# Kernel tuning notes

Hardware: AMD Instinct MI355X
Metric: run time of the kernel (lower is better)

## Reference

```python
import jax, jax.numpy as jnp
import numpy as np

B, S, D = 4, 2048, 512
H = 8
HD = D // H  # 64


def setup_inputs() -> dict:
    key = jax.random.key(0)
    k1, k2, k3 = jax.random.split(key, 3)
    x = jax.random.normal(k1, (B, S, D), dtype=jnp.float32)
    w_qkv = jax.random.normal(k2, (3 * D, D), dtype=jnp.float32) * (D ** -0.5)
    w_out = jax.random.normal(k3, (D, D), dtype=jnp.float32) * (D ** -0.5)
    return {"x": x, "w_qkv": w_qkv, "w_out": w_out}


def reference(x, w_qkv, w_out):
    b, s, d = x.shape
    # qkv projection (no bias), split into q,k,v
    qkv = jnp.einsum('bsd,ed->bse', x, w_qkv)  # [b, s, 3*d]
    q, k, v = jnp.split(qkv, 3, axis=2)
    # [b, s, h*hd] -> [b, h, s, hd]
    def to_heads(t):
        return t.reshape(b, s, H, HD).transpose(0, 2, 1, 3)
    q, k, v = to_heads(q), to_heads(k), to_heads(v)
    # NOTE: original module only scales by sqrt(head_dim) when mask is given;
    # with mask=None softmax is over raw QK^T scores.
    scores = jnp.einsum('bnid,bnjd->bnij', q, k)  # [b, h, s, s]
    attn = jax.nn.softmax(scores, axis=-1)
    o = jnp.einsum('bnij,bnjd->bnid', attn, v)  # [b, h, s, hd]
    o = o.transpose(0, 2, 1, 3).reshape(b, s, d)
    # dropout is identity (eval / drop_prob=0)
    return jnp.einsum('bsd,ed->bse', o, w_out)
```

## Files before the change

kernel.cpp:

```cpp
#include <hip/hip_runtime.h>
#include <hip/hip_bf16.h>

constexpr int B_  = 4;
constexpr int S_  = 2048;
constexpr int D_  = 512;
constexpr int H_  = 8;
constexpr int HD_ = 64;
constexpr int M_  = B_ * S_;

constexpr float LOG2E = 1.4426950408889634f;

typedef __attribute__((ext_vector_type(8))) short short8v;
typedef __attribute__((ext_vector_type(8))) _Float16 half8v;
typedef __attribute__((ext_vector_type(8))) unsigned short ushort8v;
typedef __attribute__((ext_vector_type(4))) float float4v;
typedef __attribute__((ext_vector_type(16))) float float16v;

__device__ __forceinline__ unsigned short f2bf(float x) {
    unsigned u = __builtin_bit_cast(unsigned, x);
    u += 0x7fffu + ((u >> 16) & 1u);
    return (unsigned short)(u >> 16);
}
__device__ __forceinline__ float bf2f(unsigned short h) {
    return __builtin_bit_cast(float, ((unsigned)h) << 16);
}
__device__ __forceinline__ unsigned short f2h(float x) {
    return __builtin_bit_cast(unsigned short, (_Float16)x);
}
__device__ __forceinline__ float fast_exp2(float x) {
#if __has_builtin(__builtin_amdgcn_exp2f)
    return __builtin_amdgcn_exp2f(x);
#else
    return exp2f(x);
#endif
}
__device__ __forceinline__ unsigned pack_bf16_trunc(float lo, float hi) {
    const unsigned ulo = __builtin_bit_cast(unsigned, lo);
    const unsigned uhi = __builtin_bit_cast(unsigned, hi);
#if __has_builtin(__builtin_amdgcn_perm)
    return __builtin_amdgcn_perm(uhi, ulo, 0x07060302u);
#else
    return (uhi & 0xffff0000u) | (ulo >> 16);
#endif
}
__device__ __forceinline__ void gload_lds16(const void* g, void* lds) {
    __builtin_amdgcn_global_load_lds((const __attribute__((address_space(1))) unsigned*)g,
                                     (__attribute__((address_space(3))) unsigned*)lds, 16, 0, 0);
}

__global__ __launch_bounds__(256) void prepass(const float* __restrict__ x,
                                               const float* __restrict__ wqkv,
                                               const float* __restrict__ wout,
                                               unsigned short* __restrict__ Xp,
                                               unsigned short* __restrict__ Wh,
                                               unsigned short* __restrict__ Wlq,
                                               unsigned short* __restrict__ Wob) {
    const int bid = blockIdx.x, t = threadIdx.x;
    if (bid < 2048) {
        const int flat = bid * 256 + t;
        const int m = flat >> 6, c = (flat & 63) * 8;
        const float4 a = *(const float4*)&x[(size_t)m * 512 + c];
        const float4 b = *(const float4*)&x[(size_t)m * 512 + c + 4];
        const float v[8] = {a.x, a.y, a.z, a.w, b.x, b.y, b.z, b.w};
        ushort8v hi, lo;
#pragma unroll
        for (int i = 0; i < 8; ++i) {
            const unsigned short h = f2bf(v[i]);
            hi[i] = h; lo[i] = f2bf(v[i] - bf2f(h));
        }
        *(ushort8v*)&Xp[(size_t)m * 1024 + c]       = hi;
        *(ushort8v*)&Xp[(size_t)m * 1024 + 512 + c] = lo;
    } else if (bid < 2048 + 384) {
        const int flat = (bid - 2048) * 256 + t;
        const int e = flat >> 6, c = (flat & 63) * 8;
        const float4 a = *(const float4*)&wqkv[(size_t)e * 512 + c];
        const float4 b = *(const float4*)&wqkv[(size_t)e * 512 + c + 4];
        const float v[8] = {a.x, a.y, a.z, a.w, b.x, b.y, b.z, b.w};
        ushort8v hi, lo;
#pragma unroll
        for (int i = 0; i < 8; ++i) {
            const unsigned short h = f2bf(v[i]);
            hi[i] = h; lo[i] = f2bf(v[i] - bf2f(h));
        }
        *(ushort8v*)&Wh[(size_t)e * 512 + c] = hi;
        if (e < 512) *(ushort8v*)&Wlq[(size_t)e * 512 + c] = lo;
    } else {
        const int flat = (bid - 2432) * 256 + t;
        const int e = flat >> 6, c = (flat & 63) * 8;
        const float4 a = *(const float4*)&wout[(size_t)e * 512 + c];
        const float4 b = *(const float4*)&wout[(size_t)e * 512 + c + 4];
        const float v[8] = {a.x, a.y, a.z, a.w, b.x, b.y, b.z, b.w};
        ushort8v hi;
#pragma unroll
        for (int i = 0; i < 8; ++i) hi[i] = f2bf(v[i]);
        *(ushort8v*)&Wob[(size_t)e * 512 + c] = hi;
    }
}

__global__ __launch_bounds__(256, 3) void gemm_qkv(const unsigned short* __restrict__ Xp,
                                                   const unsigned short* __restrict__ Wh,
                                                   const unsigned short* __restrict__ Wlq,
                                                   unsigned short* __restrict__ Qf,
                                                   unsigned short* __restrict__ KH,
                                                   unsigned short* __restrict__ VT) {
    __shared__ unsigned short Asm[2][128 * 64];
    __shared__ unsigned short Bsm[2][64 * 64];
    const int t = threadIdx.x, wv = t >> 6, lane = t & 63;
    const int fm = lane & 15, fq = lane >> 4;
    const int bid0 = blockIdx.x + 24 * blockIdx.y;
    const int xcd = bid0 & 7, ii = bid0 >> 3;
    const int x  = ii % 24;
    const int m0 = ((ii / 24) * 8 + xcd) * 128;
    const int slice = x >> 3;
    const int e0 = (x & 7) * 64;
    const bool vblk = (slice == 2);
    const int kiters = (slice == 0) ? 24 : 8;
    const int wrow = (wv >> 1) * 64, wcol = (wv & 1) * 32;

    const unsigned short* BbaseWh =
        Wh + (size_t)(e0 + (slice == 1 ? 512 : (slice == 2 ? 1024 : 0))) * 512;
    const unsigned short* BbaseWlq = Wlq + (size_t)e0 * 512;

    const int srow = t >> 3;
    const int skb0 = t & 7;

    float4v acc[4][2];
#pragma unroll
    for (int i = 0; i < 4; ++i)
#pragma unroll
        for (int j = 0; j < 2; ++j) acc[i][j] = (float4v){0.f, 0.f, 0.f, 0.f};

    {
#pragma unroll
        for (int i = 0; i < 4; ++i) {
            const int row = srow + 32 * i;
            const int kb = skb0 ^ (row & 7);
            gload_lds16(Xp + (size_t)(m0 + row) * 1024 + kb * 8,
                        &Asm[0][(wv * 64 + 256 * i) * 8]);
        }
#pragma unroll
        for (int i = 0; i < 2; ++i) {
            const int row = srow + 32 * i;
            const int kb = skb0 ^ (row & 7);
            gload_lds16(BbaseWh + (size_t)row * 512 + kb * 8,
                        &Bsm[0][(wv * 64 + 256 * i) * 8]);
        }
    }

    for (int kk = 0; kk < kiters; ++kk) {
        __syncthreads();

        if (kk + 1 < kiters) {
            const int nk = kk + 1;
            const int pass = nk >> 3;
            const int k0n = (nk & 7) * 64;
            const int nbuf = nk & 1;
            const int aoff = (slice == 0 && pass == 1) ? 512 : 0;
            const unsigned short* Bp = (slice == 0 && pass == 2) ? BbaseWlq : BbaseWh;
#pragma unroll
            for (int i = 0; i < 4; ++i) {
                const int row = srow + 32 * i;
                const int kb = skb0 ^ (row & 7);
                gload_lds16(Xp + (size_t)(m0 + row) * 1024 + aoff + k0n + kb * 8,
                            &Asm[nbuf][(wv * 64 + 256 * i) * 8]);
            }
#pragma unroll
            for (int i = 0; i < 2; ++i) {
                const int row = srow + 32 * i;
                const int kb = skb0 ^ (row & 7);
                gload_lds16(Bp + (size_t)row * 512 + k0n + kb * 8,
                            &Bsm[nbuf][(wv * 64 + 256 * i) * 8]);
            }
        }

        const int buf = kk & 1;
#pragma unroll
        for (int ks = 0; ks < 2; ++ks) {
            short8v af[4], bf[2];
#pragma unroll
            for (int mt = 0; mt < 4; ++mt) {
                const int row = wrow + mt * 16 + fm;
                af[mt] = *(const short8v*)&Asm[buf][row * 64 + 8 * ((4 * ks + fq) ^ (row & 7))];
            }
#pragma unroll
            for (int nt = 0; nt < 2; ++nt) {
                const int row = wcol + nt * 16 + fm;
                bf[nt] = *(const short8v*)&Bsm[buf][row * 64 + 8 * ((4 * ks + fq) ^ (row & 7))];
            }
            if (vblk) {
#pragma unroll
                for (int mt = 0; mt < 4; ++mt)
#pragma unroll
                    for (int nt = 0; nt < 2; ++nt)
                        acc[mt][nt] = __builtin_amdgcn_mfma_f32_16x16x32_bf16(bf[nt], af[mt], acc[mt][nt], 0, 0, 0);
            } else {
#pragma unroll
                for (int mt = 0; mt < 4; ++mt)
#pragma unroll
                    for (int nt = 0; nt < 2; ++nt)
                        acc[mt][nt] = __builtin_amdgcn_mfma_f32_16x16x32_bf16(af[mt], bf[nt], acc[mt][nt], 0, 0, 0);
            }
        }
    }

    if (!vblk) {
        unsigned short* __restrict__ dst = (slice == 0) ? Qf : KH;
        const float sc = (slice == 0) ? LOG2E : 1.0f;
#pragma unroll
        for (int mt = 0; mt < 4; ++mt)
#pragma unroll
            for (int nt = 0; nt < 2; ++nt) {
                const int e = e0 + wcol + nt * 16 + fm;
                const int h = e >> 6, hd = e & 63;
#pragma unroll
                for (int r = 0; r < 4; ++r) {
                    const int m = m0 + wrow + mt * 16 + 4 * fq + r;
                    const int b = m >> 11, s = m & 2047;
                    dst[((size_t)(b * 8 + h) * 2048 + s) * 64 + hd] =
                        f2h(acc[mt][nt][r] * sc);
                }
            }
    } else {
#pragma unroll
        for (int nt = 0; nt < 2; ++nt)
#pragma unroll
            for (int r = 0; r < 4; ++r) {
                const int e = e0 + wcol + nt * 16 + 4 * fq + r;
                const int h = e >> 6, hd = e & 63;
#pragma unroll
                for (int mt = 0; mt < 4; ++mt) {
                    const int m = m0 + wrow + mt * 16 + fm;
                    const int b = m >> 11, s = m & 2047;
                    const int s2 = (s & ~12) | ((s & 4) << 1) | ((s & 8) >> 1);
                    VT[((size_t)(b * 8 + h) * 64 + hd) * 2048 + s2] = f2bf(acc[mt][nt][r]);
                }
            }
    }
}

__global__ __launch_bounds__(256, 2) void attn(const unsigned short* __restrict__ Qfp,
                                               const unsigned short* __restrict__ KHp,
                                               const unsigned short* __restrict__ VTp,
                                               unsigned short* __restrict__ OB) {
    __shared__ unsigned short Ks[2][64 * 64];
    __shared__ unsigned short Vs[2][64 * 64];
    const int t = threadIdx.x, wv = t >> 6, lane = t & 63;
    const int lq = lane & 31;
    const int hf2 = lane >> 5;
    const int bid0 = blockIdx.x + 16 * blockIdx.y;
    const int xcd = bid0 & 7, ii = bid0 >> 3;
    const int bh = (ii & 3) * 8 + xcd;
    const int q0 = (ii >> 2) * 128;

    const unsigned short* qfp = Qfp + (size_t)bh * S_ * 64;
    const unsigned short* kh  = KHp + (size_t)bh * S_ * 64;
    const unsigned short* vt  = VTp + (size_t)bh * 64 * S_;

    const int srow = t >> 3;
    const int skb0 = t & 7;

#define STAGE_K(N, B) do {                                                      \
    _Pragma("unroll")                                                           \
    for (int i_ = 0; i_ < 2; ++i_) {                                            \
        const int row_ = srow + 32 * i_;                                        \
        const int kb_ = skb0 ^ (row_ & 7);                                      \
        gload_lds16(kh + (size_t)((N) * 64 + row_) * 64 + kb_ * 8,              \
                    &Ks[B][(wv * 64 + 256 * i_) * 8]);                          \
    } } while (0)

#define STAGE_V(N, B) do {                                                      \
    _Pragma("unroll")                                                           \
    for (int i_ = 0; i_ < 2; ++i_) {                                            \
        const int row_ = srow + 32 * i_;                                        \
        const int kb_ = skb0 ^ (row_ & 7);                                      \
        gload_lds16(vt + (size_t)row_ * S_ + (N) * 64 + kb_ * 8,                \
                    &Vs[B][(wv * 64 + 256 * i_) * 8]);                          \
    } } while (0)

#define QK_STEP(SN, KR) do {                                                    \
    _Pragma("unroll")                                                           \
    for (int jb_ = 0; jb_ < 2; ++jb_)                                           \
        _Pragma("unroll")                                                       \
        for (int r_ = 0; r_ < 16; ++r_) SN[jb_][r_] = 0.f;                      \
    _Pragma("unroll")                                                           \
    for (int kk_ = 0; kk_ < 4; ++kk_)                                           \
        _Pragma("unroll")                                                       \
        for (int jb_ = 0; jb_ < 2; ++jb_) {                                     \
            const int row_ = jb_ * 32 + lq;                                     \
            const int cb_ = 2 * kk_ + hf2;                                      \
            const half8v kf_ = *(const half8v*)&Ks[KR][row_ * 64 + 8 * (cb_ ^ (row_ & 7))]; \
            SN[jb_] = __builtin_amdgcn_mfma_f32_32x32x16_f16(kf_, qf[kk_], SN[jb_], 0, 0, 0); \
        } } while (0)

#define SOFTMAX_PV(SC, VR) do {                                                 \
    unsigned pk_[2][4][2];                                                      \
    _Pragma("unroll")                                                           \
    for (int jb_ = 0; jb_ < 2; ++jb_)                                           \
        _Pragma("unroll")                                                       \
        for (int g_ = 0; g_ < 4; ++g_) {                                        \
            const float p0_ = fast_exp2(SC[jb_][4 * g_ + 0]);                   \
            const float p1_ = fast_exp2(SC[jb_][4 * g_ + 1]);                   \
            const float p2_ = fast_exp2(SC[jb_][4 * g_ + 2]);                   \
            const float p3_ = fast_exp2(SC[jb_][4 * g_ + 3]);                   \
            lsum += (p0_ + p1_) + (p2_ + p3_);                                  \
            pk_[jb_][g_][0] = pack_bf16_trunc(p0_, p1_);                        \
            pk_[jb_][g_][1] = pack_bf16_trunc(p2_, p3_);                        \
        }                                                                       \
    __builtin_amdgcn_s_setprio(1);                                              \
    _Pragma("unroll")                                                           \
    for (int jc_ = 0; jc_ < 4; ++jc_) {                                         \
        const int jb_ = jc_ >> 1, gg_ = (jc_ & 1) * 2;                          \
        const uint4 uu_ = {pk_[jb_][gg_][0], pk_[jb_][gg_][1],                  \
                           pk_[jb_][gg_ + 1][0], pk_[jb_][gg_ + 1][1]};         \
        const short8v pa_ = __builtin_bit_cast(short8v, uu_);                   \
        _Pragma("unroll")                                                       \
        for (int db_ = 0; db_ < 2; ++db_) {                                     \
            const int vrow_ = db_ * 32 + lq;                                    \
            const int cb_ = 2 * jc_ + hf2;                                      \
            const short8v vf_ = *(const short8v*)&Vs[VR][vrow_ * 64 + 8 * (cb_ ^ (vrow_ & 7))]; \
            accO[db_] = __builtin_amdgcn_mfma_f32_32x32x16_bf16(pa_, vf_, accO[db_], 0, 0, 0);  \
        }                                                                       \
    }                                                                           \
    __builtin_amdgcn_s_setprio(0);                                              \
} while (0)

    STAGE_K(0, 0);
    STAGE_V(0, 0);
    STAGE_K(1, 1);

    half8v qf[4];
    {
        const int qrow = q0 + wv * 32 + lq;
#pragma unroll
        for (int kk = 0; kk < 4; ++kk)
            qf[kk] = *(const half8v*)&qfp[(size_t)qrow * 64 + kk * 16 + hf2 * 8];
    }

    float16v accO[2];
#pragma unroll
    for (int db = 0; db < 2; ++db)
#pragma unroll
        for (int r = 0; r < 16; ++r) accO[db][r] = 0.f;
    float lsum = 0.f;

    float16v sA[2], sB[2];

    __syncthreads();
    QK_STEP(sA, 0);
    __syncthreads();

    for (int jt = 0; jt < 32; jt += 2) {
        if (jt + 2 < 32) STAGE_K(jt + 2, 0);
        STAGE_V(jt + 1, 1);
        QK_STEP(sB, 1);
        SOFTMAX_PV(sA, 0);
        __syncthreads();
        if (jt + 3 < 32) STAGE_K(jt + 3, 1);
        if (jt + 2 < 32) {
            STAGE_V(jt + 2, 0);
            QK_STEP(sA, 0);
        }
        SOFTMAX_PV(sB, 1);
        __syncthreads();
    }

#undef STAGE_K
#undef STAGE_V
#undef QK_STEP
#undef SOFTMAX_PV

    const float ls = lsum + __shfl_xor(lsum, 32);
    const float invl = 1.f / ls;

    const int b = bh >> 3, hh = bh & 7;
#pragma unroll
    for (int g = 0; g < 4; ++g)
#pragma unroll
        for (int r = 0; r < 4; ++r) {
            const int qrow = r + 8 * g + 4 * hf2;
            const float inv = __shfl(invl, qrow);
            const int q = q0 + wv * 32 + qrow;
#pragma unroll
            for (int db = 0; db < 2; ++db)
                OB[((size_t)(b * 2048 + q)) * 512 + hh * 64 + db * 32 + lq] =
                    f2bf(accO[db][4 * g + r] * inv);
        }
}

__global__ __launch_bounds__(256) void gemm_out(const unsigned short* __restrict__ OB,
                                                const unsigned short* __restrict__ Wob,
                                                float* __restrict__ out) {
    __shared__ unsigned short Asm[2][128 * 64];
    __shared__ unsigned short Bsm[2][64 * 64];
    const int t = threadIdx.x, wv = t >> 6, lane = t & 63;
    const int fm = lane & 15, fq = lane >> 4;
    const int bid0 = blockIdx.x + 8 * blockIdx.y;
    const int xcd = bid0 & 7, ii = bid0 >> 3;
    const int e0 = (ii % 8) * 64;
    const int m0 = ((ii / 8) * 8 + xcd) * 128;
    const int wrow = (wv & 1) * 64, wcol = (wv >> 1) * 32;

    const int srow = t >> 3;
    const int skb0 = t & 7;

    float4v acc[4][2];
#pragma unroll
    for (int i = 0; i < 4; ++i)
#pragma unroll
        for (int j = 0; j < 2; ++j) acc[i][j] = (float4v){0.f, 0.f, 0.f, 0.f};

#pragma unroll
    for (int i = 0; i < 4; ++i) {
        const int row = srow + 32 * i;
        const int kb = skb0 ^ (row & 7);
        gload_lds16(OB + (size_t)(m0 + row) * 512 + kb * 8,
                    &Asm[0][(wv * 64 + 256 * i) * 8]);
    }
#pragma unroll
    for (int i = 0; i < 2; ++i) {
        const int row = srow + 32 * i;
        const int kb = skb0 ^ (row & 7);
        gload_lds16(Wob + (size_t)(e0 + row) * 512 + kb * 8,
                    &Bsm[0][(wv * 64 + 256 * i) * 8]);
    }

    for (int kk = 0; kk < 8; ++kk) {
        __syncthreads();
        if (kk + 1 < 8) {
            const int k0n = (kk + 1) * 64, nbuf = (kk + 1) & 1;
#pragma unroll
            for (int i = 0; i < 4; ++i) {
                const int row = srow + 32 * i;
                const int kb = skb0 ^ (row & 7);
                gload_lds16(OB + (size_t)(m0 + row) * 512 + k0n + kb * 8,
                            &Asm[nbuf][(wv * 64 + 256 * i) * 8]);
            }
#pragma unroll
            for (int i = 0; i < 2; ++i) {
                const int row = srow + 32 * i;
                const int kb = skb0 ^ (row & 7);
                gload_lds16(Wob + (size_t)(e0 + row) * 512 + k0n + kb * 8,
                            &Bsm[nbuf][(wv * 64 + 256 * i) * 8]);
            }
        }
        const int buf = kk & 1;
#pragma unroll
        for (int ks = 0; ks < 2; ++ks) {
            short8v af[4], bf[2];
#pragma unroll
            for (int mt = 0; mt < 4; ++mt) {
                const int row = wrow + mt * 16 + fm;
                af[mt] = *(const short8v*)&Asm[buf][row * 64 + 8 * ((4 * ks + fq) ^ (row & 7))];
            }
#pragma unroll
            for (int nt = 0; nt < 2; ++nt) {
                const int row = wcol + nt * 16 + fm;
                bf[nt] = *(const short8v*)&Bsm[buf][row * 64 + 8 * ((4 * ks + fq) ^ (row & 7))];
            }
#pragma unroll
            for (int mt = 0; mt < 4; ++mt)
#pragma unroll
                for (int nt = 0; nt < 2; ++nt)
                    acc[mt][nt] = __builtin_amdgcn_mfma_f32_16x16x32_bf16(af[mt], bf[nt], acc[mt][nt], 0, 0, 0);
        }
    }
#pragma unroll
    for (int mt = 0; mt < 4; ++mt)
#pragma unroll
        for (int nt = 0; nt < 2; ++nt)
#pragma unroll
            for (int r = 0; r < 4; ++r) {
                const int m = m0 + wrow + mt * 16 + 4 * fq + r;
                const int e = e0 + wcol + nt * 16 + fm;
                out[(size_t)m * 512 + e] = acc[mt][nt][r];
            }
}

extern "C" void kernel_launch(void* const* d_in, const int* in_sizes, int n_in,
                              void* d_out, int out_size, void* d_ws, size_t ws_size,
                              hipStream_t stream) {
    const float* x     = (const float*)d_in[0];
    const float* w_qkv = (const float*)d_in[1];
    const float* w_out = (const float*)d_in[2];
    float* out = (float*)d_out;

    char* p = (char*)d_ws;
    unsigned short* Xp  = (unsigned short*)p;  p += (size_t)M_ * 1024 * 2;
    unsigned short* Wh  = (unsigned short*)p;  p += (size_t)1536 * 512 * 2;
    unsigned short* Wlq = (unsigned short*)p;  p += (size_t)512 * 512 * 2;
    unsigned short* Wob = (unsigned short*)p;  p += (size_t)512 * 512 * 2;
    unsigned short* Qf  = (unsigned short*)p;  p += (size_t)32 * S_ * 64 * 2;
    unsigned short* KH  = (unsigned short*)p;  p += (size_t)32 * S_ * 64 * 2;
    unsigned short* VT  = (unsigned short*)p;  p += (size_t)32 * 64 * S_ * 2;
    unsigned short* OB  = Xp;

    prepass<<<2560, 256, 0, stream>>>(x, w_qkv, w_out, Xp, Wh, Wlq, Wob);
    gemm_qkv<<<dim3(24, 64), 256, 0, stream>>>(Xp, Wh, Wlq, Qf, KH, VT);
    attn<<<dim3(16, 32), 256, 0, stream>>>(Qf, KH, VT, OB);
    gemm_out<<<dim3(8, 64), 256, 0, stream>>>(OB, Wob, out);
}
```

Before: 162.2 us.

## Process two query sub-tiles per wave in attention to reuse K/V fragments

Each attention wave now handles 64 query rows (two 32-row sub-tiles) instead of 32, so each block covers 256 queries and the grid halves to 256 blocks. K and V fragments read from LDS are reused across both sub-tiles, halving LDS and global K/V traffic per query. The cost is doubled accumulator and score register use, with launch bounds relaxed to one block per SM. With only 256 blocks on a large GPU, occupancy and latency hiding may suffer.

```diff
diff --git a/kernel.cpp b/kernel.cpp
--- a/kernel.cpp
+++ b/kernel.cpp
@@ -238,7 +238,7 @@
     }
 }
 
-__global__ __launch_bounds__(256, 2) void attn(const unsigned short* __restrict__ Qfp,
+__global__ __launch_bounds__(256, 1) void attn(const unsigned short* __restrict__ Qfp,
                                                const unsigned short* __restrict__ KHp,
                                                const unsigned short* __restrict__ VTp,
                                                unsigned short* __restrict__ OB) {
@@ -247,10 +247,10 @@
     const int t = threadIdx.x, wv = t >> 6, lane = t & 63;
     const int lq = lane & 31;
     const int hf2 = lane >> 5;
-    const int bid0 = blockIdx.x + 16 * blockIdx.y;
+    const int bid0 = blockIdx.x + 8 * blockIdx.y;
     const int xcd = bid0 & 7, ii = bid0 >> 3;
     const int bh = (ii & 3) * 8 + xcd;
-    const int q0 = (ii >> 2) * 128;
+    const int q0 = (ii >> 2) * 256;
 
     const unsigned short* qfp = Qfp + (size_t)bh * S_ * 64;
     const unsigned short* kh  = KHp + (size_t)bh * S_ * 64;
@@ -279,9 +279,11 @@
 
 #define QK_STEP(SN, KR) do {                                                    \
     _Pragma("unroll")                                                           \
-    for (int jb_ = 0; jb_ < 2; ++jb_)                                           \
+    for (int qb_ = 0; qb_ < 2; ++qb_)                                           \
         _Pragma("unroll")                                                       \
-        for (int r_ = 0; r_ < 16; ++r_) SN[jb_][r_] = 0.f;                      \
+        for (int jb_ = 0; jb_ < 2; ++jb_)                                       \
+            _Pragma("unroll")                                                   \
+            for (int r_ = 0; r_ < 16; ++r_) SN[qb_][jb_][r_] = 0.f;             \
     _Pragma("unroll")                                                           \
     for (int kk_ = 0; kk_ < 4; ++kk_)                                           \
         _Pragma("unroll")                                                       \
@@ -289,36 +291,43 @@
             const int row_ = jb_ * 32 + lq;                                     \
             const int cb_ = 2 * kk_ + hf2;                                      \
             const half8v kf_ = *(const half8v*)&Ks[KR][row_ * 64 + 8 * (cb_ ^ (row_ & 7))]; \
-            SN[jb_] = __builtin_amdgcn_mfma_f32_32x32x16_f16(kf_, qf[kk_], SN[jb_], 0, 0, 0); \
+            SN[0][jb_] = __builtin_amdgcn_mfma_f32_32x32x16_f16(kf_, qf[0][kk_], SN[0][jb_], 0, 0, 0); \
+            SN[1][jb_] = __builtin_amdgcn_mfma_f32_32x32x16_f16(kf_, qf[1][kk_], SN[1][jb_], 0, 0, 0); \
         } } while (0)
 
 #define SOFTMAX_PV(SC, VR) do {                                                 \
-    unsigned pk_[2][4][2];                                                      \
+    unsigned pk_[2][2][4][2];                                                   \
     _Pragma("unroll")                                                           \
-    for (int jb_ = 0; jb_ < 2; ++jb_)                                           \
+    for (int qb_ = 0; qb_ < 2; ++qb_)                                           \
         _Pragma("unroll")                                                       \
-        for (int g_ = 0; g_ < 4; ++g_) {                                        \
-            const float p0_ = fast_exp2(SC[jb_][4 * g_ + 0]);                   \
-            const float p1_ = fast_exp2(SC[jb_][4 * g_ + 1]);                   \
-            const float p2_ = fast_exp2(SC[jb_][4 * g_ + 2]);                   \
-            const float p3_ = fast_exp2(SC[jb_][4 * g_ + 3]);                   \
-            lsum += (p0_ + p1_) + (p2_ + p3_);                                  \
-            pk_[jb_][g_][0] = pack_bf16_trunc(p0_, p1_);                        \
-            pk_[jb_][g_][1] = pack_bf16_trunc(p2_, p3_);                        \
-        }                                                                       \
+        for (int jb_ = 0; jb_ < 2; ++jb_)                                       \
+            _Pragma("unroll")                                                   \
+            for (int g_ = 0; g_ < 4; ++g_) {                                    \
+                const float p0_ = fast_exp2(SC[qb_][jb_][4 * g_ + 0]);          \
+                const float p1_ = fast_exp2(SC[qb_][jb_][4 * g_ + 1]);          \
+                const float p2_ = fast_exp2(SC[qb_][jb_][4 * g_ + 2]);          \
+                const float p3_ = fast_exp2(SC[qb_][jb_][4 * g_ + 3]);          \
+                lsum[qb_] += (p0_ + p1_) + (p2_ + p3_);                         \
+                pk_[qb_][jb_][g_][0] = pack_bf16_trunc(p0_, p1_);               \
+                pk_[qb_][jb_][g_][1] = pack_bf16_trunc(p2_, p3_);               \
+            }                                                                   \
     __builtin_amdgcn_s_setprio(1);                                              \
     _Pragma("unroll")                                                           \
     for (int jc_ = 0; jc_ < 4; ++jc_) {                                         \
         const int jb_ = jc_ >> 1, gg_ = (jc_ & 1) * 2;                          \
-        const uint4 uu_ = {pk_[jb_][gg_][0], pk_[jb_][gg_][1],                  \
-                           pk_[jb_][gg_ + 1][0], pk_[jb_][gg_ + 1][1]};         \
-        const short8v pa_ = __builtin_bit_cast(short8v, uu_);                   \
+        const uint4 u0_ = {pk_[0][jb_][gg_][0], pk_[0][jb_][gg_][1],            \
+                           pk_[0][jb_][gg_ + 1][0], pk_[0][jb_][gg_ + 1][1]};   \
+        const uint4 u1_ = {pk_[1][jb_][gg_][0], pk_[1][jb_][gg_][1],            \
+                           pk_[1][jb_][gg_ + 1][0], pk_[1][jb_][gg_ + 1][1]};   \
+        const short8v pa0_ = __builtin_bit_cast(short8v, u0_);                  \
+        const short8v pa1_ = __builtin_bit_cast(short8v, u1_);                  \
         _Pragma("unroll")                                                       \
         for (int db_ = 0; db_ < 2; ++db_) {                                     \
             const int vrow_ = db_ * 32 + lq;                                    \
             const int cb_ = 2 * jc_ + hf2;                                      \
             const short8v vf_ = *(const short8v*)&Vs[VR][vrow_ * 64 + 8 * (cb_ ^ (vrow_ & 7))]; \
-            accO[db_] = __builtin_amdgcn_mfma_f32_32x32x16_bf16(pa_, vf_, accO[db_], 0, 0, 0);  \
+            accO[0][db_] = __builtin_amdgcn_mfma_f32_32x32x16_bf16(pa0_, vf_, accO[0][db_], 0, 0, 0); \
+            accO[1][db_] = __builtin_amdgcn_mfma_f32_32x32x16_bf16(pa1_, vf_, accO[1][db_], 0, 0, 0); \
         }                                                                       \
     }                                                                           \
     __builtin_amdgcn_s_setprio(0);                                              \
@@ -328,22 +337,27 @@
     STAGE_V(0, 0);
     STAGE_K(1, 1);
 
-    half8v qf[4];
+    half8v qf[2][4];
     {
-        const int qrow = q0 + wv * 32 + lq;
-#pragma unroll
-        for (int kk = 0; kk < 4; ++kk)
-            qf[kk] = *(const half8v*)&qfp[(size_t)qrow * 64 + kk * 16 + hf2 * 8];
-    }
-
-    float16v accO[2];
-#pragma unroll
-    for (int db = 0; db < 2; ++db)
-#pragma unroll
-        for (int r = 0; r < 16; ++r) accO[db][r] = 0.f;
-    float lsum = 0.f;
-
-    float16v sA[2], sB[2];
+#pragma unroll
+        for (int qb = 0; qb < 2; ++qb) {
+            const int qrow = q0 + wv * 64 + qb * 32 + lq;
+#pragma unroll
+            for (int kk = 0; kk < 4; ++kk)
+                qf[qb][kk] = *(const half8v*)&qfp[(size_t)qrow * 64 + kk * 16 + hf2 * 8];
+        }
+    }
+
+    float16v accO[2][2];
+#pragma unroll
+    for (int qb = 0; qb < 2; ++qb)
+#pragma unroll
+        for (int db = 0; db < 2; ++db)
+#pragma unroll
+            for (int r = 0; r < 16; ++r) accO[qb][db][r] = 0.f;
+    float lsum[2] = {0.f, 0.f};
+
+    float16v sA[2][2], sB[2][2];
 
     __syncthreads();
     QK_STEP(sA, 0);
@@ -369,22 +383,24 @@
 #undef QK_STEP
 #undef SOFTMAX_PV
 
-    const float ls = lsum + __shfl_xor(lsum, 32);
-    const float invl = 1.f / ls;
-
     const int b = bh >> 3, hh = bh & 7;
 #pragma unroll
-    for (int g = 0; g < 4; ++g)
-#pragma unroll
-        for (int r = 0; r < 4; ++r) {
-            const int qrow = r + 8 * g + 4 * hf2;
-            const float inv = __shfl(invl, qrow);
-            const int q = q0 + wv * 32 + qrow;
-#pragma unroll
-            for (int db = 0; db < 2; ++db)
-                OB[((size_t)(b * 2048 + q)) * 512 + hh * 64 + db * 32 + lq] =
-                    f2bf(accO[db][4 * g + r] * inv);
-        }
+    for (int qb = 0; qb < 2; ++qb) {
+        const float ls = lsum[qb] + __shfl_xor(lsum[qb], 32);
+        const float invl = 1.f / ls;
+#pragma unroll
+        for (int g = 0; g < 4; ++g)
+#pragma unroll
+            for (int r = 0; r < 4; ++r) {
+                const int qrow = r + 8 * g + 4 * hf2;
+                const float inv = __shfl(invl, qrow);
+                const int q = q0 + wv * 64 + qb * 32 + qrow;
+#pragma unroll
+                for (int db = 0; db < 2; ++db)
+                    OB[((size_t)(b * 2048 + q)) * 512 + hh * 64 + db * 32 + lq] =
+                        f2bf(accO[qb][db][4 * g + r] * inv);
+            }
+    }
 }
 
 __global__ __launch_bounds__(256) void gemm_out(const unsigned short* __restrict__ OB,
@@ -496,6 +512,6 @@
 
     prepass<<<2560, 256, 0, stream>>>(x, w_qkv, w_out, Xp, Wh, Wlq, Wob);
     gemm_qkv<<<dim3(24, 64), 256, 0, stream>>>(Xp, Wh, Wlq, Qf, KH, VT);
-    attn<<<dim3(16, 32), 256, 0, stream>>>(Qf, KH, VT, OB);
+    attn<<<dim3(8, 32), 256, 0, stream>>>(Qf, KH, VT, OB);
     gemm_out<<<dim3(8, 64), 256, 0, stream>>>(OB, Wob, out);
 }
```

After: 169.0 us. 1.04x slower.

## Split attention KV range across two blocks and merge partials in a combine kernel

Applied to the files above, without the earlier changes.

The attention kernel now splits the 32 key tiles into two halves, handled by separate blocks, which doubles the grid to 1024 blocks. The occupancy hint goes from 2 to 4 blocks per CU. Each block writes unnormalized fp32 partial outputs and row sums to workspace, and a new combine kernel adds the two halves, normalizes, and writes bf16 for the output GEMM. The aim is more parallelism and latency hiding in attention. The cost is extra fp32 partial traffic, an additional launch, and possible register pressure from the tighter launch bound.

```diff
diff --git a/kernel.cpp b/kernel.cpp
--- a/kernel.cpp
+++ b/kernel.cpp
@@ -238,23 +238,31 @@
     }
 }
 
-__global__ __launch_bounds__(256, 2) void attn(const unsigned short* __restrict__ Qfp,
+__global__ __launch_bounds__(256, 4) void attn(const unsigned short* __restrict__ Qfp,
                                                const unsigned short* __restrict__ KHp,
                                                const unsigned short* __restrict__ VTp,
-                                               unsigned short* __restrict__ OB) {
+                                               float* __restrict__ Op0,
+                                               float* __restrict__ Op1,
+                                               float* __restrict__ Lp0,
+                                               float* __restrict__ Lp1) {
     __shared__ unsigned short Ks[2][64 * 64];
     __shared__ unsigned short Vs[2][64 * 64];
     const int t = threadIdx.x, wv = t >> 6, lane = t & 63;
     const int lq = lane & 31;
     const int hf2 = lane >> 5;
-    const int bid0 = blockIdx.x + 16 * blockIdx.y;
+    const int bid0 = blockIdx.x + 32 * blockIdx.y;
     const int xcd = bid0 & 7, ii = bid0 >> 3;
-    const int bh = (ii & 3) * 8 + xcd;
-    const int q0 = (ii >> 2) * 128;
+    const int bh = (ii >> 5) * 8 + xcd;
+    const int rr = ii & 31;
+    const int q0 = (rr >> 1) * 128;
+    const int jh = rr & 1;
+    const int jb0 = jh * 16;
 
     const unsigned short* qfp = Qfp + (size_t)bh * S_ * 64;
     const unsigned short* kh  = KHp + (size_t)bh * S_ * 64;
     const unsigned short* vt  = VTp + (size_t)bh * 64 * S_;
+    float* __restrict__ Op = (jh ? Op1 : Op0);
+    float* __restrict__ Lp = (jh ? Lp1 : Lp0);
 
     const int srow = t >> 3;
     const int skb0 = t & 7;
@@ -324,9 +332,9 @@
     __builtin_amdgcn_s_setprio(0);                                              \
 } while (0)
 
-    STAGE_K(0, 0);
-    STAGE_V(0, 0);
-    STAGE_K(1, 1);
+    STAGE_K(jb0, 0);
+    STAGE_V(jb0, 0);
+    STAGE_K(jb0 + 1, 1);
 
     half8v qf[4];
     {
@@ -349,15 +357,15 @@
     QK_STEP(sA, 0);
     __syncthreads();
 
-    for (int jt = 0; jt < 32; jt += 2) {
-        if (jt + 2 < 32) STAGE_K(jt + 2, 0);
-        STAGE_V(jt + 1, 1);
+    for (int n = 0; n < 16; n += 2) {
+        if (n + 2 < 16) STAGE_K(jb0 + n + 2, 0);
+        STAGE_V(jb0 + n + 1, 1);
         QK_STEP(sB, 1);
         SOFTMAX_PV(sA, 0);
         __syncthreads();
-        if (jt + 3 < 32) STAGE_K(jt + 3, 1);
-        if (jt + 2 < 32) {
-            STAGE_V(jt + 2, 0);
+        if (n + 3 < 16) STAGE_K(jb0 + n + 3, 1);
+        if (n + 2 < 16) {
+            STAGE_V(jb0 + n + 2, 0);
             QK_STEP(sA, 0);
         }
         SOFTMAX_PV(sB, 1);
@@ -370,21 +378,42 @@
 #undef SOFTMAX_PV
 
     const float ls = lsum + __shfl_xor(lsum, 32);
-    const float invl = 1.f / ls;
-
-    const int b = bh >> 3, hh = bh & 7;
+    if (hf2 == 0) Lp[((size_t)bh << 11) + q0 + wv * 32 + lq] = ls;
+
+    float* op = Op + ((size_t)bh * 2048 + q0 + wv * 32) * 64;
 #pragma unroll
     for (int g = 0; g < 4; ++g)
 #pragma unroll
         for (int r = 0; r < 4; ++r) {
             const int qrow = r + 8 * g + 4 * hf2;
-            const float inv = __shfl(invl, qrow);
-            const int q = q0 + wv * 32 + qrow;
 #pragma unroll
             for (int db = 0; db < 2; ++db)
-                OB[((size_t)(b * 2048 + q)) * 512 + hh * 64 + db * 32 + lq] =
-                    f2bf(accO[db][4 * g + r] * inv);
-        }
+                op[(size_t)qrow * 64 + db * 32 + lq] = accO[db][4 * g + r];
+        }
+}
+
+__global__ __launch_bounds__(256) void combine(const float* __restrict__ Op0,
+                                               const float* __restrict__ Op1,
+                                               const float* __restrict__ Lp0,
+                                               const float* __restrict__ Lp1,
+                                               unsigned short* __restrict__ OB) {
+    const size_t idx = ((size_t)blockIdx.x * 256 + threadIdx.x) * 8;
+    const int bh = (int)(idx >> 17);
+    const int rem = (int)(idx & 131071);
+    const int q = rem >> 6, d0 = rem & 63;
+    const size_t lidx = ((size_t)bh << 11) + q;
+    const float inv = 1.f / (Lp0[lidx] + Lp1[lidx]);
+    const float4 a0 = *(const float4*)&Op0[idx];
+    const float4 a1 = *(const float4*)&Op0[idx + 4];
+    const float4 b0 = *(const float4*)&Op1[idx];
+    const float4 b1 = *(const float4*)&Op1[idx + 4];
+    const float v[8] = {a0.x + b0.x, a0.y + b0.y, a0.z + b0.z, a0.w + b0.w,
+                        a1.x + b1.x, a1.y + b1.y, a1.z + b1.z, a1.w + b1.w};
+    ushort8v o;
+#pragma unroll
+    for (int i = 0; i < 8; ++i) o[i] = f2bf(v[i] * inv);
+    const int b = bh >> 3, h = bh & 7;
+    *(ushort8v*)&OB[((size_t)(b * 2048 + q)) * 512 + h * 64 + d0] = o;
 }
 
 __global__ __launch_bounds__(256) void gemm_out(const unsigned short* __restrict__ OB,
@@ -492,10 +521,15 @@
     unsigned short* Qf  = (unsigned short*)p;  p += (size_t)32 * S_ * 64 * 2;
     unsigned short* KH  = (unsigned short*)p;  p += (size_t)32 * S_ * 64 * 2;
     unsigned short* VT  = (unsigned short*)p;  p += (size_t)32 * 64 * S_ * 2;
-    unsigned short* OB  = Xp;
+    float* Op1          = (float*)p;           p += (size_t)32 * S_ * 64 * 4;
+    float* Op0 = (float*)Xp;
+    float* Lp0 = (float*)Wh;
+    float* Lp1 = Lp0 + (size_t)32 * S_;
+    unsigned short* OB = Qf;
 
     prepass<<<2560, 256, 0, stream>>>(x, w_qkv, w_out, Xp, Wh, Wlq, Wob);
     gemm_qkv<<<dim3(24, 64), 256, 0, stream>>>(Xp, Wh, Wlq, Qf, KH, VT);
-    attn<<<dim3(16, 32), 256, 0, stream>>>(Qf, KH, VT, OB);
+    attn<<<dim3(32, 32), 256, 0, stream>>>(Qf, KH, VT, Op0, Op1, Lp0, Lp1);
+    combine<<<2048, 256, 0, stream>>>(Op0, Op1, Lp0, Lp1, OB);
     gemm_out<<<dim3(8, 64), 256, 0, stream>>>(OB, Wob, out);
 }
```

Result: slower. 282.8 us (+74.4%).
